# Kernel tuning notes

Measured on AMD Instinct MI355X. Metric: run time of the kernel, lower is better.

Reference implementation:

```python
import jax, jax.numpy as jnp
import numpy as np


def setup_inputs() -> dict:
    key = jax.random.key(0)
    k1, k2, k3 = jax.random.split(key, 3)
    B, C, H, W = 4, 256, 64, 64
    K = max(C // 16, 8)  # 16
    x = jax.random.normal(k1, (B, C, H, W), dtype=jnp.float32)
    # conv1: 1x1 conv C -> K, i.e. a channel matmul with bias
    w1 = jax.random.normal(k2, (K, C), dtype=jnp.float32) * (1.0 / np.sqrt(C))
    b1 = jax.random.normal(k3, (K,), dtype=jnp.float32) * 0.01
    return {"x": x, "w1": w1, "b1": b1}


def reference(x, w1, b1):
    B, C, H, W = x.shape
    N = H * W
    xf = x.reshape(B, C, N)                       # [B, C, N]
    # conv1(x) flattened: proj used as both query and key (same weights)
    f = jnp.einsum('kc,bcn->bkn', w1, xf) + b1[None, :, None]  # [B, K, N]
    # energy[b, n, m] = sum_k f[b,k,n] * f[b,k,m]
    energy = jnp.einsum('bkn,bkm->bnm', f, f)     # [B, N, N]
    attention = jax.nn.softmax(energy, axis=-1)   # softmax over m
    # out[b,c,n] = sum_m value[b,c,m] * attention[b,n,m]
    out = jnp.einsum('bcm,bnm->bcn', xf, attention)
    out = out.reshape(B, C, H, W)
    return x + out * 0.1
```

## Files before the change

### kernel.cpp

```cpp
#include <hip/hip_runtime.h>
#include <hip/hip_bf16.h>

#define B_ 4
#define C_ 256
#define N_ 4096
#define K_ 16
#define QB 64
#define FSCALE 1.2011224087864498f
#define EXPA 8388608.0f
#define EXPB 1065101558.0f

typedef float f32x4 __attribute__((ext_vector_type(4)));
typedef float f32x16 __attribute__((ext_vector_type(16)));
typedef short s16x8 __attribute__((ext_vector_type(8)));
typedef int   i32x4 __attribute__((ext_vector_type(4)));
typedef int   i32x2 __attribute__((ext_vector_type(2)));

__device__ __forceinline__ short f2bf(float f) {
  union { float f; unsigned u; } v; v.f = f;
  unsigned r = v.u + 0x7fffu + ((v.u >> 16) & 1u);
  return (short)(r >> 16);
}
__device__ __forceinline__ int packbf(float a, float b) {
  __hip_bfloat162 h = __float22bfloat162_rn(make_float2(a, b));
  int r; __builtin_memcpy(&r, &h, 4); return r;
}

__global__ __launch_bounds__(256) void pre(const float* __restrict__ x,
                                           const float* __restrict__ w1,
                                           const float* __restrict__ b1,
                                           short* __restrict__ fT,
                                           short* __restrict__ vtP) {
  __shared__ __align__(16) char sm[20480];
  const int tid = threadIdx.x;
  if (blockIdx.x < 512) {
    float* w1t = (float*)sm;
    __shared__ float pr[8][32][17];
    for (int i = tid; i < C_ * K_; i += 256) {
      int k = i >> 8, c = i & 255;
      w1t[c * K_ + k] = w1[i];
    }
    __syncthreads();
    const int blk = blockIdx.x;
    const int b = blk >> 7;
    const int n0 = (blk & 127) * 32;
    const int nl = tid & 31;
    const int cch = tid >> 5;
    const int n = n0 + nl;
    const float* xp = x + (size_t)b * C_ * N_ + n;
    float acc[K_];
#pragma unroll
    for (int k = 0; k < K_; k++) acc[k] = 0.f;
    for (int cc = 0; cc < 32; cc++) {
      int c = cch * 32 + cc;
      float v = xp[(size_t)c * N_];
      const f32x4* wp = (const f32x4*)(&w1t[c * K_]);
#pragma unroll
      for (int qq = 0; qq < 4; qq++) {
        f32x4 wv = wp[qq];
#pragma unroll
        for (int j = 0; j < 4; j++) acc[qq * 4 + j] += wv[j] * v;
      }
    }
#pragma unroll
    for (int k = 0; k < K_; k++) pr[cch][nl][k] = acc[k];
    __syncthreads();
#pragma unroll
    for (int jj = 0; jj < 2; jj++) {
      int o = tid + jj * 256;
      int on = o >> 4, ok = o & 15;
      float s = b1[ok];
#pragma unroll
      for (int u = 0; u < 8; u++) s += pr[u][on][ok];
      fT[((size_t)b * N_ + n0 + on) * K_ + ok] = f2bf(s * FSCALE);
    }
  } else {
    short* t = (short*)sm;
    const int bid = blockIdx.x - 512;
    const int b = bid >> 7, cb = (bid >> 5) & 3, nb = bid & 31;
    const int n0 = nb * 128, c0 = cb * 64;
    const int r = tid >> 2, cg = tid & 3;
    const float* xp = x + ((size_t)(b * 256 + c0 + r)) * N_ + n0 + cg * 32;
#pragma unroll
    for (int k = 0; k < 8; k++) {
      f32x4 v = *(const f32x4*)(xp + k * 4);
      i32x2 p = {packbf(v[0], v[1]), packbf(v[2], v[3])};
      int col = (cg * 32 + k * 4) ^ ((r & 7) * 8);
      *(i32x2*)(&t[r * 136 + col]) = p;
    }
    __syncthreads();
#pragma unroll
    for (int u = 0; u < 4; u++) {
      int chunk = tid + 256 * u;
      int gl = chunk >> 6, c = chunk & 63;
      int m16 = gl >> 1, hi = gl & 1;
      int swz = (c & 7) * 8;
      i32x2 a = *(const i32x2*)(&t[c * 136 + ((m16 * 16 + hi * 4) ^ swz)]);
      i32x2 bq = *(const i32x2*)(&t[c * 136 + ((m16 * 16 + 8 + hi * 4) ^ swz)]);
      i32x4 vv = {a[0], a[1], bq[0], bq[1]};
      size_t g = (size_t)b * 512 + (size_t)(nb * 8 + m16) * 2 + hi;
      *(i32x4*)(vtP + (g * 256 + c0 + c) * 8) = vv;
    }
  }
}

__global__ __launch_bounds__(1024) void flash16(const float* __restrict__ x,
                                                const short* __restrict__ vtP,
                                                const short* __restrict__ fT,
                                                float* __restrict__ out) {
  __shared__ __align__(16) char lds[65536];
  const int tid = threadIdx.x;
  const int l = tid & 63;
  const int w = tid >> 6;
  const int h = w >> 3;
  const int u = w & 7;
  const int mt_p = u >> 1;
  const int nt_p = u & 1;
  const int hi = l >> 5;
  const int q = l & 31;
  const int id = blockIdx.x;
  const int b = id & 3;
  const int n0 = (id >> 2) * QB;

  const short* fTb = fT + (size_t)b * N_ * K_;
  const int mh0 = h * 2048;

  const s16x8 qf = *(const s16x8*)(fTb + (size_t)(n0 + nt_p * 32 + q) * K_ + hi * 8);
  const short* pkb = fTb + (size_t)(mh0 + mt_p * 64 + q) * K_ + hi * 8;
  const short* pvb = vtP + (((size_t)b * 512 + (mh0 >> 4) * 2 + hi) * 256 + u * 32 + q) * 8;

  char* pwr = lds + ((h * 2 + nt_p) * 4 + mt_p) * 4096 + hi * 512 + q * 16;
  const int prdO = hi * 512 + q * 16;

  f32x16 zero16 = {};
  f32x16 acc0 = zero16, acc1 = zero16;
  float lrun = 0.f;

  s16x8 kf0 = *(const s16x8*)(pkb);
  s16x8 kf1 = *(const s16x8*)(pkb + 32 * K_);

  for (int si = 0; si < 8; ++si) {
    __builtin_amdgcn_s_setprio(1);
    f32x16 st0 = __builtin_amdgcn_mfma_f32_32x32x16_bf16(kf0, qf, zero16, 0, 0, 0);
    f32x16 st1 = __builtin_amdgcn_mfma_f32_32x32x16_bf16(kf1, qf, zero16, 0, 0, 0);

    const short* pkn = pkb + (size_t)((si < 7 ? si + 1 : 7) * 256) * K_;
    s16x8 nk0 = *(const s16x8*)(pkn);
    s16x8 nk1 = *(const s16x8*)(pkn + 32 * K_);

    int sd0[8], sd1[8];
    float ps0 = 0.f, ps1 = 0.f, ps2 = 0.f, ps3 = 0.f;
#pragma unroll
    for (int s2 = 0; s2 < 8; s2++) {
      int ia = (int)(st0[2 * s2] * EXPA + EXPB);
      int ib = (int)(st0[2 * s2 + 1] * EXPA + EXPB);
      ps0 += __int_as_float(ia);
      ps1 += __int_as_float(ib);
      sd0[s2] = (int)__builtin_amdgcn_perm((unsigned)ib, (unsigned)ia, 0x07060302u);
    }
#pragma unroll
    for (int s2 = 0; s2 < 8; s2++) {
      int ia = (int)(st1[2 * s2] * EXPA + EXPB);
      int ib = (int)(st1[2 * s2 + 1] * EXPA + EXPB);
      ps2 += __int_as_float(ia);
      ps3 += __int_as_float(ib);
      sd1[s2] = (int)__builtin_amdgcn_perm((unsigned)ib, (unsigned)ia, 0x07060302u);
    }
    lrun += (ps0 + ps1) + (ps2 + ps3);
    __builtin_amdgcn_s_setprio(0);

    *(i32x4*)(pwr)        = (i32x4){sd0[0], sd0[1], sd0[2], sd0[3]};
    *(i32x4*)(pwr + 1024) = (i32x4){sd0[4], sd0[5], sd0[6], sd0[7]};
    *(i32x4*)(pwr + 2048) = (i32x4){sd1[0], sd1[1], sd1[2], sd1[3]};
    *(i32x4*)(pwr + 3072) = (i32x4){sd1[4], sd1[5], sd1[6], sd1[7]};
    __syncthreads();

    __builtin_amdgcn_s_setprio(1);
#pragma unroll
    for (int mt = 0; mt < 4; ++mt) {
      const short* pv = pvb + (size_t)(si * 4 + mt) * 16384;
      s16x8 vA0 = *(const s16x8*)(pv);
      s16x8 vA1 = *(const s16x8*)(pv + 4096);
      s16x8 vA2 = *(const s16x8*)(pv + 8192);
      s16x8 vA3 = *(const s16x8*)(pv + 12288);
      const char* p0 = lds + ((h * 2 + 0) * 4 + mt) * 4096 + prdO;
      const char* p1 = lds + ((h * 2 + 1) * 4 + mt) * 4096 + prdO;
      s16x8 pa0 = __builtin_bit_cast(s16x8, *(const i32x4*)(p0));
      s16x8 pb0 = __builtin_bit_cast(s16x8, *(const i32x4*)(p1));
      acc0 = __builtin_amdgcn_mfma_f32_32x32x16_bf16(vA0, pa0, acc0, 0, 0, 0);
      acc1 = __builtin_amdgcn_mfma_f32_32x32x16_bf16(vA0, pb0, acc1, 0, 0, 0);
      s16x8 pa1 = __builtin_bit_cast(s16x8, *(const i32x4*)(p0 + 1024));
      s16x8 pb1 = __builtin_bit_cast(s16x8, *(const i32x4*)(p1 + 1024));
      acc0 = __builtin_amdgcn_mfma_f32_32x32x16_bf16(vA1, pa1, acc0, 0, 0, 0);
      acc1 = __builtin_amdgcn_mfma_f32_32x32x16_bf16(vA1, pb1, acc1, 0, 0, 0);
      s16x8 pa2 = __builtin_bit_cast(s16x8, *(const i32x4*)(p0 + 2048));
      s16x8 pb2 = __builtin_bit_cast(s16x8, *(const i32x4*)(p1 + 2048));
      acc0 = __builtin_amdgcn_mfma_f32_32x32x16_bf16(vA2, pa2, acc0, 0, 0, 0);
      acc1 = __builtin_amdgcn_mfma_f32_32x32x16_bf16(vA2, pb2, acc1, 0, 0, 0);
      s16x8 pa3 = __builtin_bit_cast(s16x8, *(const i32x4*)(p0 + 3072));
      s16x8 pb3 = __builtin_bit_cast(s16x8, *(const i32x4*)(p1 + 3072));
      acc0 = __builtin_amdgcn_mfma_f32_32x32x16_bf16(vA3, pa3, acc0, 0, 0, 0);
      acc1 = __builtin_amdgcn_mfma_f32_32x32x16_bf16(vA3, pb3, acc1, 0, 0, 0);
    }
    __builtin_amdgcn_s_setprio(0);
    __syncthreads();

    kf0 = nk0; kf1 = nk1;
  }

  lrun += __shfl_xor(lrun, 32);

  float* mlb = (float*)lds;
  mlb[w * 64 + l] = lrun;
  __syncthreads();
  float L0 = 0.f, L1 = 0.f;
#pragma unroll
  for (int hh = 0; hh < 2; ++hh)
#pragma unroll
    for (int mt = 0; mt < 4; ++mt) {
      L0 += mlb[(hh * 8 + mt * 2 + 0) * 64 + l];
      L1 += mlb[(hh * 8 + mt * 2 + 1) * 64 + l];
    }
  __syncthreads();
  char* xch = lds;
  const int xbase = (u * 64 + l) * 128;
  if (h == 1) {
#pragma unroll
    for (int i = 0; i < 8; i++) {
      f32x4 v;
#pragma unroll
      for (int r = 0; r < 4; r++) v[r] = (i >> 2) ? acc1[(i & 3) * 4 + r] : acc0[(i & 3) * 4 + r];
      *(f32x4*)(xch + xbase + ((i * 16) ^ ((l & 7) << 4))) = v;
    }
  }
  __syncthreads();
  if (h == 0) {
    const float inv0 = 0.1f / L0;
    const float inv1 = 0.1f / L1;
#pragma unroll
    for (int i = 0; i < 8; i++) {
      f32x4 po = *(const f32x4*)(xch + xbase + ((i * 16) ^ ((l & 7) << 4)));
      const int p_ = i & 3;
      const int ntw = i >> 2;
      const float inv = ntw ? inv1 : inv0;
      const int n = n0 + ntw * 32 + q;
      const int cbase = u * 32 + p_ * 8 + hi * 4;
#pragma unroll
      for (int r = 0; r < 4; r++) {
        const float own = ntw ? acc1[p_ * 4 + r] : acc0[p_ * 4 + r];
        const size_t idx = ((size_t)b * C_ + (cbase + r)) * N_ + n;
        out[idx] = x[idx] + (own + po[r]) * inv;
      }
    }
  }
}

extern "C" void kernel_launch(void* const* d_in, const int* in_sizes, int n_in,
                              void* d_out, int out_size, void* d_ws, size_t ws_size,
                              hipStream_t stream) {
  const float* x  = (const float*)d_in[0];
  const float* w1 = (const float*)d_in[1];
  const float* b1 = (const float*)d_in[2];
  float* out = (float*)d_out;
  short* fT  = (short*)d_ws;
  short* vtP = (short*)((char*)d_ws + 512 * 1024);
  pre<<<dim3(1024), dim3(256), 0, stream>>>(x, w1, b1, fT, vtP);
  flash16<<<dim3(256), dim3(1024), 0, stream>>>(x, vtP, fT, out);
}
```

Before: 61.41 us.

## Software-pipeline QK softmax of next tile with PV MFMAs of current tile

Computes the first tile's scores and exp-probabilities before the loop. Inside the loop it computes the next tile's QK MFMAs and exponentials while the current tile's PV MFMAs run from LDS. The new probabilities are written to LDS after a barrier, with the last iteration's redundant work masked out of the row sum. The aim is to overlap exp/VALU work with matrix-core work. The cost is an extra barrier per iteration, more live registers, and one wasted tile of score compute.

```diff
diff --git a/kernel.cpp b/kernel.cpp
--- a/kernel.cpp
+++ b/kernel.cpp
@@ -104,7 +104,7 @@
   }
 }
 
-__global__ __launch_bounds__(1024) void flash16(const float* __restrict__ x,
+__global__ __launch_bounds__(1024) void flash17(const float* __restrict__ x,
                                                 const short* __restrict__ vtP,
                                                 const short* __restrict__ fT,
                                                 float* __restrict__ out) {
@@ -136,18 +136,11 @@
   f32x16 acc0 = zero16, acc1 = zero16;
   float lrun = 0.f;
 
-  s16x8 kf0 = *(const s16x8*)(pkb);
-  s16x8 kf1 = *(const s16x8*)(pkb + 32 * K_);
-
-  for (int si = 0; si < 8; ++si) {
-    __builtin_amdgcn_s_setprio(1);
-    f32x16 st0 = __builtin_amdgcn_mfma_f32_32x32x16_bf16(kf0, qf, zero16, 0, 0, 0);
-    f32x16 st1 = __builtin_amdgcn_mfma_f32_32x32x16_bf16(kf1, qf, zero16, 0, 0, 0);
-
-    const short* pkn = pkb + (size_t)((si < 7 ? si + 1 : 7) * 256) * K_;
-    s16x8 nk0 = *(const s16x8*)(pkn);
-    s16x8 nk1 = *(const s16x8*)(pkn + 32 * K_);
-
+  {
+    s16x8 k0 = *(const s16x8*)(pkb);
+    s16x8 k1 = *(const s16x8*)(pkb + 32 * K_);
+    f32x16 st0 = __builtin_amdgcn_mfma_f32_32x32x16_bf16(k0, qf, zero16, 0, 0, 0);
+    f32x16 st1 = __builtin_amdgcn_mfma_f32_32x32x16_bf16(k1, qf, zero16, 0, 0, 0);
     int sd0[8], sd1[8];
     float ps0 = 0.f, ps1 = 0.f, ps2 = 0.f, ps3 = 0.f;
 #pragma unroll
@@ -167,15 +160,45 @@
       sd1[s2] = (int)__builtin_amdgcn_perm((unsigned)ib, (unsigned)ia, 0x07060302u);
     }
     lrun += (ps0 + ps1) + (ps2 + ps3);
-    __builtin_amdgcn_s_setprio(0);
-
     *(i32x4*)(pwr)        = (i32x4){sd0[0], sd0[1], sd0[2], sd0[3]};
     *(i32x4*)(pwr + 1024) = (i32x4){sd0[4], sd0[5], sd0[6], sd0[7]};
     *(i32x4*)(pwr + 2048) = (i32x4){sd1[0], sd1[1], sd1[2], sd1[3]};
     *(i32x4*)(pwr + 3072) = (i32x4){sd1[4], sd1[5], sd1[6], sd1[7]};
-    __syncthreads();
+  }
+  __syncthreads();
+  s16x8 kf0 = *(const s16x8*)(pkb + 256 * K_);
+  s16x8 kf1 = *(const s16x8*)(pkb + 256 * K_ + 32 * K_);
+
+  for (int si = 0; si < 8; ++si) {
+    const float lsc = (si < 7) ? 1.f : 0.f;
+    const short* pkn = pkb + (size_t)((si + 2 < 7 ? si + 2 : 7) * 256) * K_;
 
     __builtin_amdgcn_s_setprio(1);
+
+    f32x16 st0 = __builtin_amdgcn_mfma_f32_32x32x16_bf16(kf0, qf, zero16, 0, 0, 0);
+    f32x16 st1 = __builtin_amdgcn_mfma_f32_32x32x16_bf16(kf1, qf, zero16, 0, 0, 0);
+    s16x8 nk0 = *(const s16x8*)(pkn);
+    s16x8 nk1 = *(const s16x8*)(pkn + 32 * K_);
+    int sd0[8], sd1[8];
+    float ps0 = 0.f, ps1 = 0.f, ps2 = 0.f, ps3 = 0.f;
+#pragma unroll
+    for (int s2 = 0; s2 < 8; s2++) {
+      int ia = (int)(st0[2 * s2] * EXPA + EXPB);
+      int ib = (int)(st0[2 * s2 + 1] * EXPA + EXPB);
+      ps0 += __int_as_float(ia);
+      ps1 += __int_as_float(ib);
+      sd0[s2] = (int)__builtin_amdgcn_perm((unsigned)ib, (unsigned)ia, 0x07060302u);
+    }
+#pragma unroll
+    for (int s2 = 0; s2 < 8; s2++) {
+      int ia = (int)(st1[2 * s2] * EXPA + EXPB);
+      int ib = (int)(st1[2 * s2 + 1] * EXPA + EXPB);
+      ps2 += __int_as_float(ia);
+      ps3 += __int_as_float(ib);
+      sd1[s2] = (int)__builtin_amdgcn_perm((unsigned)ib, (unsigned)ia, 0x07060302u);
+    }
+    lrun += lsc * ((ps0 + ps1) + (ps2 + ps3));
+
 #pragma unroll
     for (int mt = 0; mt < 4; ++mt) {
       const short* pv = pvb + (size_t)(si * 4 + mt) * 16384;
@@ -205,6 +228,12 @@
     __builtin_amdgcn_s_setprio(0);
     __syncthreads();
 
+    *(i32x4*)(pwr)        = (i32x4){sd0[0], sd0[1], sd0[2], sd0[3]};
+    *(i32x4*)(pwr + 1024) = (i32x4){sd0[4], sd0[5], sd0[6], sd0[7]};
+    *(i32x4*)(pwr + 2048) = (i32x4){sd1[0], sd1[1], sd1[2], sd1[3]};
+    *(i32x4*)(pwr + 3072) = (i32x4){sd1[4], sd1[5], sd1[6], sd1[7]};
+    __syncthreads();
+
     kf0 = nk0; kf1 = nk1;
   }
 
@@ -265,5 +294,5 @@
   short* fT  = (short*)d_ws;
   short* vtP = (short*)((char*)d_ws + 512 * 1024);
   pre<<<dim3(1024), dim3(256), 0, stream>>>(x, w1, b1, fT, vtP);
-  flash16<<<dim3(256), dim3(1024), 0, stream>>>(x, vtP, fT, out);
-}
+  flash17<<<dim3(256), dim3(1024), 0, stream>>>(x, vtP, fT, out);
+}
```

Result: no change. 61.38 us (-0.0%).
